# Kernel optimization log

Measured on AMD Instinct MI355X. Metric: run time of the kernel, lower is better.

Reference implementation:

```python
import jax, jax.numpy as jnp
import numpy as np

D_MODEL = 1024
N_HEADS = 16
HEAD_DIM = D_MODEL // N_HEADS
ROPE_BASE = 10000.0
EPS = 1e-5


def _rope_cos_sin(seq_len, dtype):
    inv_freq = 1.0 / (ROPE_BASE ** (jnp.arange(0, HEAD_DIM, 2, dtype=jnp.float32) / HEAD_DIM))
    t = jnp.arange(seq_len, dtype=jnp.float32)
    freqs = jnp.einsum('i,j->ij', t, inv_freq)          # [S, HEAD_DIM/2]
    emb = jnp.concatenate([freqs, freqs], axis=-1)      # [S, HEAD_DIM]
    return jnp.cos(emb).astype(dtype), jnp.sin(emb).astype(dtype)


def _rotate_half(x):
    x1, x2 = jnp.split(x, 2, axis=-1)
    return jnp.concatenate([-x2, x1], axis=-1)


def _apply_rope(x, cos, sin):
    # x: [B, S, H, Dh]; cos/sin: [S, Dh] -> broadcast [1, S, 1, Dh]
    cos = cos[None, :, None, :]
    sin = sin[None, :, None, :]
    return x * cos + _rotate_half(x) * sin


def setup_inputs() -> dict:
    key = jax.random.key(0)
    ks = jax.random.split(key, 6)
    B, Td, Te = 4, 2048, 2048
    s = 1.0 / np.sqrt(D_MODEL)
    return {
        'x': jax.random.normal(ks[0], (B, Td, D_MODEL), jnp.float32),
        'encoder_out': jax.random.normal(ks[1], (B, Te, D_MODEL), jnp.float32),
        'norm_w': jnp.ones((D_MODEL,), jnp.float32),
        'Wq': jax.random.normal(ks[2], (D_MODEL, D_MODEL), jnp.float32) * s,
        'Wkv': jax.random.normal(ks[3], (2 * D_MODEL, D_MODEL), jnp.float32) * s,
        'Wo': jax.random.normal(ks[4], (D_MODEL, D_MODEL), jnp.float32) * s,
    }


def reference(x, encoder_out, norm_w, Wq, Wkv, Wo):
    B, Td, _ = x.shape
    Te = encoder_out.shape[1]
    residual = x
    # RMSNorm
    rms = jax.lax.rsqrt(jnp.mean(x * x, axis=-1, keepdims=True) + EPS)
    xn = x * rms * norm_w
    # Projections (nn.Linear: y = x @ W.T)
    q = (xn @ Wq.T).reshape(B, Td, N_HEADS, HEAD_DIM)
    kv = (encoder_out @ Wkv.T).reshape(B, Te, 2, N_HEADS, HEAD_DIM)
    k, v = kv[:, :, 0], kv[:, :, 1]
    # RoPE (q_offset=0, k_offset=0)
    cos, sin = _rope_cos_sin(max(Td, Te), q.dtype)
    q = _apply_rope(q, cos[:Td], sin[:Td])
    k = _apply_rope(k, cos[:Te], sin[:Te])
    # SDPA cross-attention (non-causal)
    scale = 1.0 / jnp.sqrt(jnp.asarray(HEAD_DIM, q.dtype))
    scores = jnp.einsum('bqhd,bkhd->bhqk', q, k) * scale
    attn = jax.nn.softmax(scores, axis=-1)
    out = jnp.einsum('bhqk,bkhd->bqhd', attn, v).reshape(B, Td, D_MODEL)
    out = out @ Wo.T
    return residual + out
```

## Files before the change

kernel.cpp:

```cpp
#include <hip/hip_runtime.h>
#include <cstdint>


#define DEVI __device__ __forceinline__

typedef float f32x4 __attribute__((ext_vector_type(4)));
typedef float f32x16 __attribute__((ext_vector_type(16)));
typedef __bf16 bf16x8 __attribute__((ext_vector_type(8)));
typedef unsigned u32x2 __attribute__((ext_vector_type(2)));

DEVI unsigned short f2bf(float f) {
  union { float f; unsigned u; } v; v.f = f;
  unsigned r = v.u + 0x7FFFu + ((v.u >> 16) & 1u);
  return (unsigned short)(r >> 16);
}
DEVI f32x4 mfma16(bf16x8 a, bf16x8 b, f32x4 c) {
  return __builtin_amdgcn_mfma_f32_16x16x32_bf16(a, b, c, 0, 0, 0);
}
DEVI f32x16 mfma32(bf16x8 a, bf16x8 b, f32x16 c) {
  return __builtin_amdgcn_mfma_f32_32x32x16_bf16(a, b, c, 0, 0, 0);
}
DEVI void gl_lds16(const void* g, void* l) {
  __builtin_amdgcn_global_load_lds((const __attribute__((address_space(1))) void*)g,
                                   (__attribute__((address_space(3))) void*)l,
                                   16, 0, 0);
}
DEVI unsigned cvtpk_bf16(float lo, float hi) {
  unsigned r;
  asm("v_cvt_pk_bf16_f32 %0, %1, %2" : "=v"(r) : "v"(lo), "v"(hi));
  return r;
}
DEVI float xhalf(float x, int hi) {
  union { float f; unsigned u; } a; a.f = x;
  u32x2 r = __builtin_amdgcn_permlane32_swap(a.u, a.u, false, false);
  union { unsigned u; float f; } o; o.u = hi ? r.x : r.y;
  return o.f;
}


__global__ void conv_bf16_k(const float* __restrict__ in, unsigned short* __restrict__ out, long n4) {
  long i = (long)blockIdx.x * blockDim.x + threadIdx.x;
  if (i >= n4) return;
  const float4 v = ((const float4*)in)[i];
  ushort4 o;
  o.x = f2bf(v.x); o.y = f2bf(v.y); o.z = f2bf(v.z); o.w = f2bf(v.w);
  ((ushort4*)out)[i] = o;
}

__global__ void rmsnorm_k(const float* __restrict__ x, const float* __restrict__ wgt,
                          unsigned short* __restrict__ xn) {
  const int row = blockIdx.x;
  const int t = threadIdx.x;
  const float4 v = ((const float4*)(x + (long)row * 1024))[t];
  float ss = v.x * v.x + v.y * v.y + v.z * v.z + v.w * v.w;
#pragma unroll
  for (int m = 1; m < 64; m <<= 1) ss += __shfl_xor(ss, m, 64);
  __shared__ float red[4];
  if ((t & 63) == 0) red[t >> 6] = ss;
  __syncthreads();
  const float tot = red[0] + red[1] + red[2] + red[3];
  const float rms = rsqrtf(tot * (1.f / 1024.f) + 1e-5f);
  const float4 wv = ((const float4*)wgt)[t];
  ushort4 o;
  o.x = f2bf(v.x * rms * wv.x);
  o.y = f2bf(v.y * rms * wv.y);
  o.z = f2bf(v.z * rms * wv.z);
  o.w = f2bf(v.w * rms * wv.w);
  ((ushort4*)(xn + (long)row * 1024))[t] = o;
}

__global__ void rope_tab_k(float* __restrict__ tab) {
  const int i = blockIdx.x * 256 + threadIdx.x;
  const int j = i >> 11, t = i & 2047;
  const float inv = powf(10000.f, -(float)j * (1.f / 32.f));
  const float a = (float)t * inv;
  tab[i] = cosf(a);
  tab[65536 + i] = sinf(a);
}

template <int EPI>
__launch_bounds__(256, 2)
__global__ void gemm_bt_k(const unsigned short* __restrict__ A,
                          const unsigned short* __restrict__ Bw,
                          unsigned short* __restrict__ o_bf0,
                          unsigned short* __restrict__ o_bf1,
                          float* __restrict__ o_f32,
                          const float* __restrict__ resid,
                          const float* __restrict__ cosT,
                          const float* __restrict__ sinT,
                          float scl, int N, int K) {
  __shared__ unsigned short As[2][128 * 32];
  __shared__ unsigned short Bs[2][128 * 32];
  const int tix = threadIdx.x;
  const int w = tix >> 6, l = tix & 63;
  const int wr = w >> 1, wc = w & 1;
  const int lr = l & 15, lg = l >> 4;
  const long bm = blockIdx.y, bn = blockIdx.x;
  const long arow0 = bm * 128, brow0 = bn * 128;

  f32x4 acc[4][4] = {};

  const int r2 = tix >> 2, c2 = tix & 3;
  const int sw2 = c2 ^ (r2 & 3);

  auto stage = [&](int buf, int kt) {
    const long k0 = (long)kt * 32;
    const unsigned short* ga  = A  + (arow0 + r2) * K + k0 + sw2 * 8;
    const unsigned short* ga2 = A  + (arow0 + 64 + r2) * K + k0 + sw2 * 8;
    const unsigned short* gb  = Bw + (brow0 + r2) * K + k0 + sw2 * 8;
    const unsigned short* gb2 = Bw + (brow0 + 64 + r2) * K + k0 + sw2 * 8;
    char* la = (char*)&As[buf][0] + w * 1024;
    char* lb = (char*)&Bs[buf][0] + w * 1024;
    gl_lds16(ga,  la);
    gl_lds16(ga2, la + 4096);
    gl_lds16(gb,  lb);
    gl_lds16(gb2, lb + 4096);
  };

  auto lds_off = [&](int row, int chunk) { return row * 32 + ((chunk ^ (row & 3)) << 3); };

  auto compute = [&](int buf) {
    bf16x8 af[4], bv[4];
#pragma unroll
    for (int m = 0; m < 4; ++m)
      af[m] = *(const bf16x8*)&As[buf][lds_off(wr * 64 + m * 16 + lr, lg)];
#pragma unroll
    for (int n = 0; n < 4; ++n)
      bv[n] = *(const bf16x8*)&Bs[buf][lds_off(wc * 64 + n * 16 + lr, lg)];
#pragma unroll
    for (int m = 0; m < 4; ++m)
#pragma unroll
      for (int n = 0; n < 4; ++n)
        acc[m][n] = mfma16(af[m], bv[n], acc[m][n]);
  };

  const int nk = K >> 5;
  stage(0, 0);
  __syncthreads();
  int buf = 0;
#pragma unroll 1
  for (int kt = 0; kt < nk - 1; ++kt) {
    stage(buf ^ 1, kt + 1);
    compute(buf);
    __syncthreads();
    buf ^= 1;
  }
  compute(buf);

  if constexpr (EPI == 2) {
#pragma unroll
    for (int m = 0; m < 4; ++m)
#pragma unroll
      for (int n = 0; n < 4; ++n)
#pragma unroll
        for (int r = 0; r < 4; ++r) {
          const long grow = arow0 + wr * 64 + m * 16 + lg * 4 + r;
          const long gcol = brow0 + wc * 64 + n * 16 + lr;
          const long idx = grow * 1024 + gcol;
          o_f32[idx] = acc[m][n][r] + resid[idx];
        }
    return;
  }

  const long b = arow0 >> 11;
  const bool isV = (EPI == 1) && (brow0 >= 1024);
  const long colbase = isV ? (brow0 - 1024 + wc * 64) : (brow0 + wc * 64);
  const long hh = (colbase >> 6) & 15;
  const long bh = b * 16 + hh;

#pragma unroll
  for (int m = 0; m < 4; ++m) {
    const long tt0 = (arow0 + wr * 64 + m * 16 + lg * 4) & 2047;
    if (!isV) {
      const float4 c0 = *(const float4*)(cosT + (long)lr * 2048 + tt0);
      const float4 s0 = *(const float4*)(sinT + (long)lr * 2048 + tt0);
      const float4 c1 = *(const float4*)(cosT + (long)(16 + lr) * 2048 + tt0);
      const float4 s1 = *(const float4*)(sinT + (long)(16 + lr) * 2048 + tt0);
      const int hi_ = (lr >> 3) & 1, j_ = lr & 7;
#pragma unroll
      for (int r = 0; r < 4; ++r) {
        const long tt = tt0 + r;
        const long base = (((bh * 64 + (tt >> 5)) * 4 + 0) * 64 + hi_ * 32 + (tt & 31)) * 8 + j_;
        const float a0 = acc[m][0][r], a1 = acc[m][1][r], a2 = acc[m][2][r], a3 = acc[m][3][r];
        const float cc0 = ((const float*)&c0)[r], ss0 = ((const float*)&s0)[r];
        const float cc1 = ((const float*)&c1)[r], ss1 = ((const float*)&s1)[r];
        o_bf0[base]        = f2bf((a0 * cc0 - a2 * ss0) * scl);
        o_bf0[base + 512]  = f2bf((a1 * cc1 - a3 * ss1) * scl);
        o_bf0[base + 1024] = f2bf((a2 * cc0 + a0 * ss0) * scl);
        o_bf0[base + 1536] = f2bf((a3 * cc1 + a1 * ss1) * scl);
      }
    } else {
#pragma unroll
      for (int r = 0; r < 4; ++r) {
        const long tt = tt0 + r;
        const long kt = tt >> 5, kv5 = tt & 31;
        const long viL = kv5 >> 4, hi_ = (kv5 >> 3) & 1, jj = kv5 & 7;
        const long base = (((bh * 64 + kt) * 4 + viL) * 64 + hi_ * 32 + lr) * 8 + jj;
        o_bf1[base]              = f2bf(acc[m][0][r]);
        o_bf1[base + 128]        = f2bf(acc[m][1][r]);
        o_bf1[base + 1024]       = f2bf(acc[m][2][r]);
        o_bf1[base + 1024 + 128] = f2bf(acc[m][3][r]);
      }
    }
  }
  (void)N;
}

__launch_bounds__(256, 4)
__global__ void attn_k(const unsigned short* __restrict__ Qf,
                       const unsigned short* __restrict__ Kf,
                       const unsigned short* __restrict__ Vf,
                       unsigned short* __restrict__ aout) {
  __shared__ unsigned short KLDS[2][2048];
  __shared__ unsigned short VLDS[2][2048];
  const int tix = threadIdx.x;
  const int w = tix >> 6, l = tix & 63;
  const int l31 = l & 31, hi = l >> 5;
  const int bid = blockIdx.x;
  const int bh = bid & 63, qc = bid >> 6;
  const long b = bh >> 4, h = bh & 15;
  const int q0 = qc * 128 + w * 32;
  const int qt = (q0 >> 5);

  const unsigned short* Qb = Qf + (long)bh * 131072;
  const unsigned short* Kb = Kf + (long)bh * 131072;
  const unsigned short* Vb = Vf + (long)bh * 131072;

  bf16x8 qf[4];
#pragma unroll
  for (int t = 0; t < 4; ++t)
    qf[t] = *(const bf16x8*)(Qb + ((long)qt * 4 + t) * 512 + l * 8);

  f32x16 o0 = {}, o1 = {};
  float m = -INFINITY, lsum = 0.f;

  auto stage = [&](int buf, int kt) {
    const unsigned short* gk = Kb + (long)kt * 2048 + tix * 8;
    const unsigned short* gv = Vb + (long)kt * 2048 + tix * 8;
    gl_lds16(gk, (char*)&KLDS[buf][0] + w * 1024);
    gl_lds16(gv, (char*)&VLDS[buf][0] + w * 1024);
  };

  auto process = [&](int buf) {
    bf16x8 kf0 = *(const bf16x8*)&KLDS[buf][0 * 512 + l * 8];
    bf16x8 kf1 = *(const bf16x8*)&KLDS[buf][1 * 512 + l * 8];
    bf16x8 kf2 = *(const bf16x8*)&KLDS[buf][2 * 512 + l * 8];
    bf16x8 kf3 = *(const bf16x8*)&KLDS[buf][3 * 512 + l * 8];

    f32x16 s = {};
    __builtin_amdgcn_s_setprio(1);
    s = mfma32(kf0, qf[0], s);
    s = mfma32(kf1, qf[1], s);
    s = mfma32(kf2, qf[2], s);
    s = mfma32(kf3, qf[3], s);
    __builtin_amdgcn_s_setprio(0);

    bf16x8 vf0 = *(const bf16x8*)&VLDS[buf][0 * 512 + l * 8];
    bf16x8 vf1 = *(const bf16x8*)&VLDS[buf][1 * 512 + l * 8];
    bf16x8 vf2 = *(const bf16x8*)&VLDS[buf][2 * 512 + l * 8];
    bf16x8 vf3 = *(const bf16x8*)&VLDS[buf][3 * 512 + l * 8];

    float m0 = fmaxf(fmaxf(s[0], s[1]), s[2]);
    float m1 = fmaxf(fmaxf(s[3], s[4]), s[5]);
    float m2 = fmaxf(fmaxf(s[6], s[7]), s[8]);
    float m3 = fmaxf(fmaxf(s[9], s[10]), s[11]);
    float m4 = fmaxf(fmaxf(s[12], s[13]), s[14]);
    float tm = fmaxf(fmaxf(fmaxf(m0, m1), m2), fmaxf(fmaxf(m3, m4), s[15]));
    tm = fmaxf(tm, xhalf(tm, hi));

    if (__any(tm > m + 8.f)) {
      const float mn = fmaxf(m, tm);
      const float al = exp2f(m - mn);
      m = mn;
      lsum *= al;
#pragma unroll
      for (int i = 0; i < 16; ++i) { o0[i] *= al; o1[i] *= al; }
    }

#pragma unroll
    for (int i = 0; i < 16; ++i) s[i] = exp2f(s[i] - m);
    float t0 = (s[0] + s[1]) + (s[2] + s[3]);
    float t1 = (s[4] + s[5]) + (s[6] + s[7]);
    float t2 = (s[8] + s[9]) + (s[10] + s[11]);
    float t3 = (s[12] + s[13]) + (s[14] + s[15]);
    float ts = (t0 + t1) + (t2 + t3);
    lsum += ts + xhalf(ts, hi);

    unsigned W0 = cvtpk_bf16(s[0], s[1]),   W1 = cvtpk_bf16(s[2], s[3]);
    unsigned W2 = cvtpk_bf16(s[4], s[5]),   W3 = cvtpk_bf16(s[6], s[7]);
    unsigned W4 = cvtpk_bf16(s[8], s[9]),   W5 = cvtpk_bf16(s[10], s[11]);
    unsigned W6 = cvtpk_bf16(s[12], s[13]), W7 = cvtpk_bf16(s[14], s[15]);
    const u32x2 r02 = __builtin_amdgcn_permlane32_swap(W0, W2, false, false);
    const u32x2 r13 = __builtin_amdgcn_permlane32_swap(W1, W3, false, false);
    const u32x2 r46 = __builtin_amdgcn_permlane32_swap(W4, W6, false, false);
    const u32x2 r57 = __builtin_amdgcn_permlane32_swap(W5, W7, false, false);
    unsigned af0w[4] = { r02.x, r13.x, r02.y, r13.y };
    unsigned af1w[4] = { r46.x, r57.x, r46.y, r57.y };
    const bf16x8 af0 = *(const bf16x8*)af0w;
    const bf16x8 af1 = *(const bf16x8*)af1w;

    __builtin_amdgcn_s_setprio(1);
    o0 = mfma32(vf0, af0, o0);
    o0 = mfma32(vf1, af1, o0);
    o1 = mfma32(vf2, af0, o1);
    o1 = mfma32(vf3, af1, o1);
    __builtin_amdgcn_s_setprio(0);
  };

  stage(0, 0);
  __syncthreads();
  int buf = 0;
#pragma unroll 1
  for (int kt = 0; kt < 63; ++kt) {
    stage(buf ^ 1, kt + 1);
    process(buf);
    __syncthreads();
    buf ^= 1;
  }
  process(buf);

  const float inv = 1.f / lsum;
  unsigned short* orow = aout + ((b * 2048 + q0 + l31) * 1024 + h * 64);
#pragma unroll
  for (int rg = 0; rg < 4; ++rg) {
    ushort4 v0, v1;
    v0.x = f2bf(o0[rg * 4 + 0] * inv); v0.y = f2bf(o0[rg * 4 + 1] * inv);
    v0.z = f2bf(o0[rg * 4 + 2] * inv); v0.w = f2bf(o0[rg * 4 + 3] * inv);
    v1.x = f2bf(o1[rg * 4 + 0] * inv); v1.y = f2bf(o1[rg * 4 + 1] * inv);
    v1.z = f2bf(o1[rg * 4 + 2] * inv); v1.w = f2bf(o1[rg * 4 + 3] * inv);
    *(ushort4*)(orow + rg * 8 + hi * 4)      = v0;
    *(ushort4*)(orow + 32 + rg * 8 + hi * 4) = v1;
  }
}


extern "C" void kernel_launch(void* const* d_in, const int* in_sizes, int n_in,
                              void* d_out, int out_size, void* d_ws, size_t ws_size,
                              hipStream_t stream) {
  const float* x   = (const float*)d_in[0];
  const float* enc = (const float*)d_in[1];
  const float* nw  = (const float*)d_in[2];
  const float* Wq  = (const float*)d_in[3];
  const float* Wkv = (const float*)d_in[4];
  const float* Wo  = (const float*)d_in[5];
  float* out = (float*)d_out;
  char* ws = (char*)d_ws;
  const long MB = 1024 * 1024;
  unsigned short* xn   = (unsigned short*)(ws);
  unsigned short* encb = (unsigned short*)(ws + 16 * MB);
  unsigned short* wqb  = (unsigned short*)(ws + 32 * MB);
  unsigned short* wkvb = (unsigned short*)(ws + 34 * MB);
  unsigned short* wob  = (unsigned short*)(ws + 38 * MB);
  unsigned short* Qf   = (unsigned short*)(ws + 40 * MB);
  unsigned short* Kf   = (unsigned short*)(ws + 56 * MB);
  unsigned short* Vf   = (unsigned short*)(ws + 72 * MB);
  float* tab           = (float*)(ws + 88 * MB);
  unsigned short* aout = xn;
  const float* cosT = tab;
  const float* sinT = tab + 65536;

  conv_bf16_k<<<1024, 256, 0, stream>>>(Wq, wqb, 262144);
  conv_bf16_k<<<2048, 256, 0, stream>>>(Wkv, wkvb, 524288);
  conv_bf16_k<<<1024, 256, 0, stream>>>(Wo, wob, 262144);
  conv_bf16_k<<<8192, 256, 0, stream>>>(enc, encb, 2097152);
  rmsnorm_k<<<8192, 256, 0, stream>>>(x, nw, xn);
  rope_tab_k<<<256, 256, 0, stream>>>(tab);
  gemm_bt_k<0><<<dim3(8, 64), 256, 0, stream>>>(xn, wqb, Qf, nullptr, nullptr, nullptr,
                                                cosT, sinT, 0.18033688f, 1024, 1024);
  gemm_bt_k<1><<<dim3(16, 64), 256, 0, stream>>>(encb, wkvb, Kf, Vf, nullptr, nullptr,
                                                 cosT, sinT, 1.0f, 2048, 1024);
  attn_k<<<1024, 256, 0, stream>>>(Qf, Kf, Vf, aout);
  gemm_bt_k<2><<<dim3(8, 64), 256, 0, stream>>>(aout, wob, nullptr, nullptr, out, x,
                                                cosT, sinT, 1.0f, 1024, 1024);
  (void)in_sizes; (void)n_in; (void)out_size; (void)ws_size;
}
```

Measured before the change: 359.6 us.

## Load K/V directly to registers in attention, MFMA row sums, XCD-swizzled GEMM grid

The attention kernel drops LDS staging and block barriers. Each wave now loads K and V fragments straight from global memory into registers, double-buffering K across iterations, and the occupancy hint drops from 4 to 3. The softmax denominator is accumulated by an extra pair of MFMAs against a ones vector instead of scalar adds and a cross-lane swap, and exp2 is replaced by raw v_exp_f32. The GEMM grids become 1D with a block-index swizzle that groups tiles per XCD for L2 locality. The risk is redundant global traffic, since each wave reloads the same K/V that the 4 waves previously shared through LDS, plus extra MFMA work for the sums.

```diff
diff --git a/kernel.cpp b/kernel.cpp
--- a/kernel.cpp
+++ b/kernel.cpp
@@ -4,6 +4,7 @@
 
 #define DEVI __device__ __forceinline__
 
+typedef float f32x2 __attribute__((ext_vector_type(2)));
 typedef float f32x4 __attribute__((ext_vector_type(4)));
 typedef float f32x16 __attribute__((ext_vector_type(16)));
 typedef __bf16 bf16x8 __attribute__((ext_vector_type(8)));
@@ -29,6 +30,14 @@
   unsigned r;
   asm("v_cvt_pk_bf16_f32 %0, %1, %2" : "=v"(r) : "v"(lo), "v"(hi));
   return r;
+}
+DEVI float rexp2(float x) {
+  float r;
+  asm("v_exp_f32 %0, %1" : "=v"(r) : "v"(x));
+  return r;
+}
+DEVI f32x2 max2(f32x2 a, f32x2 b) {
+  f32x2 r; r.x = fmaxf(a.x, b.x); r.y = fmaxf(a.y, b.y); return r;
 }
 DEVI float xhalf(float x, int hi) {
   union { float f; unsigned u; } a; a.f = x;
@@ -88,14 +97,17 @@
                           const float* __restrict__ resid,
                           const float* __restrict__ cosT,
                           const float* __restrict__ sinT,
-                          float scl, int N, int K) {
+                          float scl, int nbn, int K) {
   __shared__ unsigned short As[2][128 * 32];
   __shared__ unsigned short Bs[2][128 * 32];
   const int tix = threadIdx.x;
   const int w = tix >> 6, l = tix & 63;
   const int wr = w >> 1, wc = w & 1;
   const int lr = l & 15, lg = l >> 4;
-  const long bm = blockIdx.y, bn = blockIdx.x;
+  const int nwg = gridDim.x;
+  const int cpx = nwg >> 3;
+  const int swz = ((int)blockIdx.x & 7) * cpx + ((int)blockIdx.x >> 3);
+  const long bn = swz % nbn, bm = swz / nbn;
   const long arow0 = bm * 128, brow0 = bn * 128;
 
   f32x4 acc[4][4] = {};
@@ -203,16 +215,13 @@
       }
     }
   }
-  (void)N;
-}
-
-__launch_bounds__(256, 4)
+}
+
+__launch_bounds__(256, 3)
 __global__ void attn_k(const unsigned short* __restrict__ Qf,
                        const unsigned short* __restrict__ Kf,
                        const unsigned short* __restrict__ Vf,
                        unsigned short* __restrict__ aout) {
-  __shared__ unsigned short KLDS[2][2048];
-  __shared__ unsigned short VLDS[2][2048];
   const int tix = threadIdx.x;
   const int w = tix >> 6, l = tix & 63;
   const int l31 = l & 31, hi = l >> 5;
@@ -220,7 +229,7 @@
   const int bh = bid & 63, qc = bid >> 6;
   const long b = bh >> 4, h = bh & 15;
   const int q0 = qc * 128 + w * 32;
-  const int qt = (q0 >> 5);
+  const int qt = q0 >> 5;
 
   const unsigned short* Qb = Qf + (long)bh * 131072;
   const unsigned short* Kb = Kf + (long)bh * 131072;
@@ -231,60 +240,55 @@
   for (int t = 0; t < 4; ++t)
     qf[t] = *(const bf16x8*)(Qb + ((long)qt * 4 + t) * 512 + l * 8);
 
-  f32x16 o0 = {}, o1 = {};
-  float m = -INFINITY, lsum = 0.f;
-
-  auto stage = [&](int buf, int kt) {
-    const unsigned short* gk = Kb + (long)kt * 2048 + tix * 8;
-    const unsigned short* gv = Vb + (long)kt * 2048 + tix * 8;
-    gl_lds16(gk, (char*)&KLDS[buf][0] + w * 1024);
-    gl_lds16(gv, (char*)&VLDS[buf][0] + w * 1024);
-  };
-
-  auto process = [&](int buf) {
-    bf16x8 kf0 = *(const bf16x8*)&KLDS[buf][0 * 512 + l * 8];
-    bf16x8 kf1 = *(const bf16x8*)&KLDS[buf][1 * 512 + l * 8];
-    bf16x8 kf2 = *(const bf16x8*)&KLDS[buf][2 * 512 + l * 8];
-    bf16x8 kf3 = *(const bf16x8*)&KLDS[buf][3 * 512 + l * 8];
-
+  unsigned onesw[4] = { 0x3F803F80u, 0x3F803F80u, 0x3F803F80u, 0x3F803F80u };
+  const bf16x8 ones = *(const bf16x8*)onesw;
+
+  f32x16 o0 = {}, o1 = {}, ex = {};
+  float m = -INFINITY;
+
+  bf16x8 kA[4], kB[4], vv[4];
+
+  auto loadK = [&](int kt, bf16x8* kf) {
+    const unsigned short* p = Kb + (long)kt * 2048 + l * 8;
+#pragma unroll
+    for (int f = 0; f < 4; ++f) kf[f] = *(const bf16x8*)(p + f * 512);
+  };
+  auto loadV = [&](int kt, bf16x8* vf) {
+    const unsigned short* p = Vb + (long)kt * 2048 + l * 8;
+#pragma unroll
+    for (int f = 0; f < 4; ++f) vf[f] = *(const bf16x8*)(p + f * 512);
+  };
+
+  auto process = [&](const bf16x8* kf, const bf16x8* vf) {
     f32x16 s = {};
     __builtin_amdgcn_s_setprio(1);
-    s = mfma32(kf0, qf[0], s);
-    s = mfma32(kf1, qf[1], s);
-    s = mfma32(kf2, qf[2], s);
-    s = mfma32(kf3, qf[3], s);
+    s = mfma32(kf[0], qf[0], s);
+    s = mfma32(kf[1], qf[1], s);
+    s = mfma32(kf[2], qf[2], s);
+    s = mfma32(kf[3], qf[3], s);
     __builtin_amdgcn_s_setprio(0);
 
-    bf16x8 vf0 = *(const bf16x8*)&VLDS[buf][0 * 512 + l * 8];
-    bf16x8 vf1 = *(const bf16x8*)&VLDS[buf][1 * 512 + l * 8];
-    bf16x8 vf2 = *(const bf16x8*)&VLDS[buf][2 * 512 + l * 8];
-    bf16x8 vf3 = *(const bf16x8*)&VLDS[buf][3 * 512 + l * 8];
-
-    float m0 = fmaxf(fmaxf(s[0], s[1]), s[2]);
-    float m1 = fmaxf(fmaxf(s[3], s[4]), s[5]);
-    float m2 = fmaxf(fmaxf(s[6], s[7]), s[8]);
-    float m3 = fmaxf(fmaxf(s[9], s[10]), s[11]);
-    float m4 = fmaxf(fmaxf(s[12], s[13]), s[14]);
-    float tm = fmaxf(fmaxf(fmaxf(m0, m1), m2), fmaxf(fmaxf(m3, m4), s[15]));
+    const f32x2* s2 = (const f32x2*)&s;
+    f32x2 a0 = max2(s2[0], s2[1]), a1 = max2(s2[2], s2[3]);
+    f32x2 a2 = max2(s2[4], s2[5]), a3 = max2(s2[6], s2[7]);
+    a0 = max2(a0, a1); a2 = max2(a2, a3); a0 = max2(a0, a2);
+    float tm = fmaxf(a0.x, a0.y);
     tm = fmaxf(tm, xhalf(tm, hi));
 
     if (__any(tm > m + 8.f)) {
       const float mn = fmaxf(m, tm);
-      const float al = exp2f(m - mn);
+      const float al = rexp2(m - mn);
       m = mn;
-      lsum *= al;
-#pragma unroll
-      for (int i = 0; i < 16; ++i) { o0[i] *= al; o1[i] *= al; }
+#pragma unroll
+      for (int i = 0; i < 16; ++i) { o0[i] *= al; o1[i] *= al; ex[i] *= al; }
     }
 
-#pragma unroll
-    for (int i = 0; i < 16; ++i) s[i] = exp2f(s[i] - m);
-    float t0 = (s[0] + s[1]) + (s[2] + s[3]);
-    float t1 = (s[4] + s[5]) + (s[6] + s[7]);
-    float t2 = (s[8] + s[9]) + (s[10] + s[11]);
-    float t3 = (s[12] + s[13]) + (s[14] + s[15]);
-    float ts = (t0 + t1) + (t2 + t3);
-    lsum += ts + xhalf(ts, hi);
+    f32x2* sm = (f32x2*)&s;
+    const f32x2 mm = { m, m };
+#pragma unroll
+    for (int i = 0; i < 8; ++i) sm[i] = sm[i] - mm;
+#pragma unroll
+    for (int i = 0; i < 16; ++i) s[i] = rexp2(s[i]);
 
     unsigned W0 = cvtpk_bf16(s[0], s[1]),   W1 = cvtpk_bf16(s[2], s[3]);
     unsigned W2 = cvtpk_bf16(s[4], s[5]),   W3 = cvtpk_bf16(s[6], s[7]);
@@ -300,26 +304,29 @@
     const bf16x8 af1 = *(const bf16x8*)af1w;
 
     __builtin_amdgcn_s_setprio(1);
-    o0 = mfma32(vf0, af0, o0);
-    o0 = mfma32(vf1, af1, o0);
-    o1 = mfma32(vf2, af0, o1);
-    o1 = mfma32(vf3, af1, o1);
+    o0 = mfma32(vf[0], af0, o0);
+    o0 = mfma32(vf[1], af1, o0);
+    o1 = mfma32(vf[2], af0, o1);
+    o1 = mfma32(vf[3], af1, o1);
+    ex = mfma32(ones, af0, ex);
+    ex = mfma32(ones, af1, ex);
     __builtin_amdgcn_s_setprio(0);
   };
 
-  stage(0, 0);
-  __syncthreads();
-  int buf = 0;
+  loadK(0, kA);
 #pragma unroll 1
-  for (int kt = 0; kt < 63; ++kt) {
-    stage(buf ^ 1, kt + 1);
-    process(buf);
-    __syncthreads();
-    buf ^= 1;
-  }
-  process(buf);
-
-  const float inv = 1.f / lsum;
+  for (int kt = 0; kt < 62; kt += 2) {
+    loadV(kt, vv); loadK(kt + 1, kB);
+    process(kA, vv);
+    loadV(kt + 1, vv); loadK(kt + 2, kA);
+    process(kB, vv);
+  }
+  loadV(62, vv); loadK(63, kB);
+  process(kA, vv);
+  loadV(63, vv);
+  process(kB, vv);
+
+  const float inv = 1.f / ex[0];
   unsigned short* orow = aout + ((b * 2048 + q0 + l31) * 1024 + h * 64);
 #pragma unroll
   for (int rg = 0; rg < 4; ++rg) {
@@ -365,12 +372,12 @@
   conv_bf16_k<<<8192, 256, 0, stream>>>(enc, encb, 2097152);
   rmsnorm_k<<<8192, 256, 0, stream>>>(x, nw, xn);
   rope_tab_k<<<256, 256, 0, stream>>>(tab);
-  gemm_bt_k<0><<<dim3(8, 64), 256, 0, stream>>>(xn, wqb, Qf, nullptr, nullptr, nullptr,
-                                                cosT, sinT, 0.18033688f, 1024, 1024);
-  gemm_bt_k<1><<<dim3(16, 64), 256, 0, stream>>>(encb, wkvb, Kf, Vf, nullptr, nullptr,
-                                                 cosT, sinT, 1.0f, 2048, 1024);
+  gemm_bt_k<0><<<512, 256, 0, stream>>>(xn, wqb, Qf, nullptr, nullptr, nullptr,
+                                        cosT, sinT, 0.18033688f, 8, 1024);
+  gemm_bt_k<1><<<1024, 256, 0, stream>>>(encb, wkvb, Kf, Vf, nullptr, nullptr,
+                                         cosT, sinT, 1.0f, 16, 1024);
   attn_k<<<1024, 256, 0, stream>>>(Qf, Kf, Vf, aout);
-  gemm_bt_k<2><<<dim3(8, 64), 256, 0, stream>>>(aout, wob, nullptr, nullptr, out, x,
-                                                cosT, sinT, 1.0f, 1024, 1024);
+  gemm_bt_k<2><<<512, 256, 0, stream>>>(aout, wob, nullptr, nullptr, out, x,
+                                        cosT, sinT, 1.0f, 8, 1024);
   (void)in_sizes; (void)n_in; (void)out_size; (void)ws_size;
 }
```

Measured after the change: 348.0 us. 1.03x faster.
